# Kernel tuning notes

Measured on AMD Instinct MI355X. Metric: run time of the kernel, lower is better.

Reference implementation:

```python
import jax, jax.numpy as jnp
import numpy as np

B, I, O = 2048, 512, 512

def setup_inputs() -> dict:
    key = jax.random.key(0)
    kx, kw, ks = jax.random.split(key, 3)
    x = jax.random.uniform(kx, (B, I), dtype=jnp.float32)
    # shift weight logits so sigmoid(w) ~ 0.02: keeps the length-I product
    # of implication factors away from underflow (sparse conjunction)
    w_logits = jax.random.normal(kw, (I, O), dtype=jnp.float32) - 4.0
    s_logits = jax.random.normal(ks, (I, O), dtype=jnp.float32)
    return {"x": x, "w_logits": w_logits, "s_logits": s_logits}

def reference(x, w_logits, s_logits):
    # FuzzyParam.value(): sigmoid of stored logits
    w = jax.nn.sigmoid(w_logits)   # (I, O)
    s = jax.nn.sigmoid(s_logits)   # (I, O)
    xi = x[:, :, None]             # (B, I, 1)
    # product fuzzy logic:
    #   bin_xnor(a, b) = a*b + (1-a)*(1-b)
    #   implies(a, b)  = 1 - a*(1 - b)
    #   conjoin        = prod along axis
    xnor = xi * s + (1.0 - xi) * (1.0 - s)      # (B, I, O)
    factors = 1.0 - w * (1.0 - xnor)            # (B, I, O)
    return jnp.prod(factors, axis=1)            # (B, O)
```

## Files before the change

kernel.cpp:

```cpp
#include <hip/hip_runtime.h>
#include <math.h>

#define B_DIM 2048
#define I_DIM 512
#define O_DIM 512

constexpr int LANES   = 64;
constexpr int T_O     = 4;
constexpr int O_BLK   = LANES * T_O;
constexpr int NCHUNK  = 4;
constexpr int NHALF   = 2;
constexpr int R_BLOCK = 16;
constexpr int R_HALF  = R_BLOCK / NHALF;
constexpr int QPC     = (I_DIM / 4) / NCHUNK;

__global__ __launch_bounds__(256) void setup_kernel(
    const float* __restrict__ w_logits,
    const float* __restrict__ s_logits,
    float4* __restrict__ ab4)
{
    int t  = blockIdx.x * 256 + threadIdx.x;
    int o  = t & (O_DIM - 1);
    int k  = t >> 9;
    int i0 = 2 * k;

    float zw0 = w_logits[(i0 + 0) * O_DIM + o];
    float zs0 = s_logits[(i0 + 0) * O_DIM + o];
    float zw1 = w_logits[(i0 + 1) * O_DIM + o];
    float zs1 = s_logits[(i0 + 1) * O_DIM + o];

    float w0 = 1.0f / (1.0f + expf(-zw0));
    float s0 = 1.0f / (1.0f + expf(-zs0));
    float w1 = 1.0f / (1.0f + expf(-zw1));
    float s1 = 1.0f / (1.0f + expf(-zs1));

    float4 v;
    v.x = fmaf(-w0, s0, 1.0f);
    v.y = fmaf(-w1, s1, 1.0f);
    v.z = w0 * (2.0f * s0 - 1.0f);
    v.w = w1 * (2.0f * s1 - 1.0f);
    ab4[k * O_DIM + o] = v;
}

__global__ __launch_bounds__(512, 2) void fuzzy_main(
    const float* __restrict__ x,
    const float4* __restrict__ ab4,
    float* __restrict__ out)
{
    __shared__ __align__(16) unsigned char sh_raw[NCHUNK * R_BLOCK * O_BLK * 4];
    float4 (*xs4)[I_DIM / 4] =
        reinterpret_cast<float4(*)[I_DIM / 4]>(sh_raw);
    float (*part)[R_BLOCK][O_BLK] =
        reinterpret_cast<float(*)[R_BLOCK][O_BLK]>(sh_raw);

    const int lane  = threadIdx.x;
    const int y     = __builtin_amdgcn_readfirstlane((int)threadIdx.y);
    const int chunk = y & 3;
    const int half  = y >> 2;
    const int tid   = y * LANES + lane;
    const int obase = blockIdx.x * O_BLK;
    const int b0    = blockIdx.y * R_BLOCK;
    const int rbase = half * R_HALF;
    const int qbase = chunk * QPC;

    const float4* abp = ab4 + obase + lane;

    float4 cA0[T_O], cA1[T_O], cB0[T_O], cB1[T_O];
#pragma unroll
    for (int j = 0; j < T_O; ++j) {
        cA0[j] = abp[(size_t)(2 * qbase + 0) * O_DIM + 64 * j];
        cA1[j] = abp[(size_t)(2 * qbase + 1) * O_DIM + 64 * j];
        cB0[j] = abp[(size_t)(2 * qbase + 2) * O_DIM + 64 * j];
        cB1[j] = abp[(size_t)(2 * qbase + 3) * O_DIM + 64 * j];
    }

    {
        const float4* xsrc = (const float4*)x + (size_t)b0 * (I_DIM / 4);
        float4* xdst = (float4*)sh_raw;
#pragma unroll
        for (int p = 0; p < 4; ++p)
            xdst[p * 512 + tid] = xsrc[p * 512 + tid];
    }
    __syncthreads();

    float acc[R_HALF][T_O];
#pragma unroll
    for (int r = 0; r < R_HALF; ++r)
#pragma unroll
        for (int j = 0; j < T_O; ++j) acc[r][j] = 1.0f;

    for (int qq = 0; qq < QPC; qq += 2) {
        {
            const int q = qbase + qq;
#pragma unroll
            for (int r = 0; r < R_HALF; ++r) {
                float4 xv = xs4[rbase + r][q];
#pragma unroll
                for (int j = 0; j < T_O; ++j) {
                    float f0 = fmaf(cA0[j].z, xv.x, cA0[j].x);
                    float f1 = fmaf(cA0[j].w, xv.y, cA0[j].y);
                    float f2 = fmaf(cA1[j].z, xv.z, cA1[j].x);
                    float f3 = fmaf(cA1[j].w, xv.w, cA1[j].y);
                    acc[r][j] *= (f0 * f2) * (f1 * f3);
                }
            }
#pragma unroll
            for (int j = 0; j < T_O; ++j) {
                cA0[j] = abp[(size_t)(2 * q + 4) * O_DIM + 64 * j];
                cA1[j] = abp[(size_t)(2 * q + 5) * O_DIM + 64 * j];
            }
        }
        {
            const int q = qbase + qq + 1;
#pragma unroll
            for (int r = 0; r < R_HALF; ++r) {
                float4 xv = xs4[rbase + r][q];
#pragma unroll
                for (int j = 0; j < T_O; ++j) {
                    float f0 = fmaf(cB0[j].z, xv.x, cB0[j].x);
                    float f1 = fmaf(cB0[j].w, xv.y, cB0[j].y);
                    float f2 = fmaf(cB1[j].z, xv.z, cB1[j].x);
                    float f3 = fmaf(cB1[j].w, xv.w, cB1[j].y);
                    acc[r][j] *= (f0 * f2) * (f1 * f3);
                }
            }
#pragma unroll
            for (int j = 0; j < T_O; ++j) {
                cB0[j] = abp[(size_t)(2 * q + 4) * O_DIM + 64 * j];
                cB1[j] = abp[(size_t)(2 * q + 5) * O_DIM + 64 * j];
            }
        }
    }

    __syncthreads();
#pragma unroll
    for (int r = 0; r < R_HALF; ++r)
#pragma unroll
        for (int j = 0; j < T_O; ++j)
            part[chunk][rbase + r][64 * j + lane] = acc[r][j];
    __syncthreads();
#pragma unroll
    for (int p = 0; p < 8; ++p) {
        int idx = p * 512 + tid;
        int r = idx >> 8;
        int c = idx & (O_BLK - 1);
        float v = part[0][r][c] * part[1][r][c]
                * part[2][r][c] * part[3][r][c];
        out[(size_t)(b0 + r) * O_DIM + obase + c] = v;
    }
}

extern "C" void kernel_launch(void* const* d_in, const int* in_sizes, int n_in,
                              void* d_out, int out_size, void* d_ws, size_t ws_size,
                              hipStream_t stream) {
    const float* x        = (const float*)d_in[0];
    const float* w_logits = (const float*)d_in[1];
    const float* s_logits = (const float*)d_in[2];
    float* out = (float*)d_out;
    float4* ab4 = (float4*)d_ws;

    setup_kernel<<<dim3(512), dim3(256), 0, stream>>>(w_logits, s_logits, ab4);

    fuzzy_main<<<dim3(O_DIM / O_BLK, B_DIM / R_BLOCK), dim3(LANES, NCHUNK * NHALF), 0, stream>>>(
        x, ab4, out);
}
```

Before: 92.05 us.

## Split I across eight waves with all sixteen rows per wave

Each of the eight waves now covers one eighth of the input dimension for all sixteen batch rows, where before four I-chunks were paired with two row halves. Every coefficient load from global memory is therefore reused across twice as many rows, which halves coefficient traffic per block. In exchange each wave holds twice as many accumulators, which raises register pressure under the two-blocks-per-CU launch bound. The final reduction gains an extra shared-memory pass and barrier to fold the second group of four waves into the first.

```diff
diff --git a/kernel.cpp b/kernel.cpp
--- a/kernel.cpp
+++ b/kernel.cpp
@@ -8,10 +8,8 @@
 constexpr int LANES   = 64;
 constexpr int T_O     = 4;
 constexpr int O_BLK   = LANES * T_O;
-constexpr int NCHUNK  = 4;
-constexpr int NHALF   = 2;
+constexpr int NCHUNK  = 8;
 constexpr int R_BLOCK = 16;
-constexpr int R_HALF  = R_BLOCK / NHALF;
 constexpr int QPC     = (I_DIM / 4) / NCHUNK;
 
 __global__ __launch_bounds__(256) void setup_kernel(
@@ -47,7 +45,7 @@
     const float4* __restrict__ ab4,
     float* __restrict__ out)
 {
-    __shared__ __align__(16) unsigned char sh_raw[NCHUNK * R_BLOCK * O_BLK * 4];
+    __shared__ __align__(16) unsigned char sh_raw[4 * R_BLOCK * O_BLK * 4];
     float4 (*xs4)[I_DIM / 4] =
         reinterpret_cast<float4(*)[I_DIM / 4]>(sh_raw);
     float (*part)[R_BLOCK][O_BLK] =
@@ -55,13 +53,10 @@
 
     const int lane  = threadIdx.x;
     const int y     = __builtin_amdgcn_readfirstlane((int)threadIdx.y);
-    const int chunk = y & 3;
-    const int half  = y >> 2;
     const int tid   = y * LANES + lane;
     const int obase = blockIdx.x * O_BLK;
     const int b0    = blockIdx.y * R_BLOCK;
-    const int rbase = half * R_HALF;
-    const int qbase = chunk * QPC;
+    const int qbase = y * QPC;
 
     const float4* abp = ab4 + obase + lane;
 
@@ -83,9 +78,9 @@
     }
     __syncthreads();
 
-    float acc[R_HALF][T_O];
+    float acc[R_BLOCK][T_O];
 #pragma unroll
-    for (int r = 0; r < R_HALF; ++r)
+    for (int r = 0; r < R_BLOCK; ++r)
 #pragma unroll
         for (int j = 0; j < T_O; ++j) acc[r][j] = 1.0f;
 
@@ -93,8 +88,8 @@
         {
             const int q = qbase + qq;
 #pragma unroll
-            for (int r = 0; r < R_HALF; ++r) {
-                float4 xv = xs4[rbase + r][q];
+            for (int r = 0; r < R_BLOCK; ++r) {
+                float4 xv = xs4[r][q];
 #pragma unroll
                 for (int j = 0; j < T_O; ++j) {
                     float f0 = fmaf(cA0[j].z, xv.x, cA0[j].x);
@@ -113,8 +108,8 @@
         {
             const int q = qbase + qq + 1;
 #pragma unroll
-            for (int r = 0; r < R_HALF; ++r) {
-                float4 xv = xs4[rbase + r][q];
+            for (int r = 0; r < R_BLOCK; ++r) {
+                float4 xv = xs4[r][q];
 #pragma unroll
                 for (int j = 0; j < T_O; ++j) {
                     float f0 = fmaf(cB0[j].z, xv.x, cB0[j].x);
@@ -133,11 +128,21 @@
     }
 
     __syncthreads();
+    if (y < 4) {
 #pragma unroll
-    for (int r = 0; r < R_HALF; ++r)
+        for (int r = 0; r < R_BLOCK; ++r)
 #pragma unroll
-        for (int j = 0; j < T_O; ++j)
-            part[chunk][rbase + r][64 * j + lane] = acc[r][j];
+            for (int j = 0; j < T_O; ++j)
+                part[y][r][64 * j + lane] = acc[r][j];
+    }
+    __syncthreads();
+    if (y >= 4) {
+#pragma unroll
+        for (int r = 0; r < R_BLOCK; ++r)
+#pragma unroll
+            for (int j = 0; j < T_O; ++j)
+                part[y - 4][r][64 * j + lane] *= acc[r][j];
+    }
     __syncthreads();
 #pragma unroll
     for (int p = 0; p < 8; ++p) {
@@ -161,6 +166,6 @@
 
     setup_kernel<<<dim3(512), dim3(256), 0, stream>>>(w_logits, s_logits, ab4);
 
-    fuzzy_main<<<dim3(O_DIM / O_BLK, B_DIM / R_BLOCK), dim3(LANES, NCHUNK * NHALF), 0, stream>>>(
+    fuzzy_main<<<dim3(O_DIM / O_BLK, B_DIM / R_BLOCK), dim3(LANES, NCHUNK), 0, stream>>>(
         x, ab4, out);
 }
```

Result: faster. 87.82 us (-4.6%).
